# Optimization experiments

Measured on AMD Instinct MI355X. Metric: run time of the kernel, lower is better.

The kernel has to match this reference:

```python
import jax, jax.numpy as jnp
import numpy as np

TOPK = 20

def setup_inputs() -> dict:
    key = jax.random.key(0)
    k1, k2, k3 = jax.random.split(key, 3)
    B, n, D = 4, 4096, 256
    src1 = jax.random.normal(k1, (B, n, D), dtype=jnp.float32)
    src2 = jax.random.normal(k2, (B, n, D), dtype=jnp.float32)
    memoryMartix = jax.random.normal(k3, (n, n), dtype=jnp.float32)
    return {"src1": src1, "src2": src2, "memoryMartix": memoryMartix}

def reference(src1, src2, memoryMartix):
    # softmax over dim=1 of the [n, n] memory matrix
    probs = jax.nn.softmax(memoryMartix, axis=1)            # [n, n]
    # top-k along dim=1: values and indices per row
    vtopk, ind = jax.lax.top_k(probs, TOPK)                 # [n, k], [n, k]
    # gather src2 rows per output position: [B, n, k, D]
    gathered = jnp.take(src2, ind, axis=1)
    # weighted sum over the k selected neighbors
    src = jnp.einsum('bnkd,nk->bnd', gathered, vtopk)       # [B, n, D]
    return src + src1
```

## Files before the change

kernel.cpp:

```cpp
#include <hip/hip_runtime.h>
#include <math.h>

#define TOPK  20
#define NROW  4096
#define DDIM  256
#define NB    4
#define NCHUNK 16

#define AWPB   2
#define ABLOCK (AWPB * 64)
#define BBLOCK 256

typedef float vf4 __attribute__((ext_vector_type(4)));

__device__ __forceinline__ void wave_lds_fence() {
    asm volatile("s_waitcnt lgkmcnt(0)" ::: "memory");
}

__device__ __forceinline__ bool lex_gt(float av, int ai, float bv, int bi) {
    return (av > bv) || (av == bv && ai < bi);
}

__device__ __forceinline__ void bitonic64_desc(float& v, int& i, int lane) {
#pragma unroll
    for (int k = 2; k <= 64; k <<= 1) {
#pragma unroll
        for (int j = k >> 1; j > 0; j >>= 1) {
            float pv = __shfl_xor(v, j, 64);
            int   pi = __shfl_xor(i, j, 64);
            bool takeBig = ((lane & k) == 0) == ((lane & j) == 0);
            bool pBig = lex_gt(pv, pi, v, i);
            if (takeBig == pBig) { v = pv; i = pi; }
        }
    }
}

__global__ __launch_bounds__(ABLOCK, 4) void topk_select(
    const float* __restrict__ mem,
    float* __restrict__ ws_w,
    int*   __restrict__ ws_i)
{
    __shared__ float cand_v[AWPB][64];
    __shared__ int   cand_i[AWPB][64];
    const int wave = threadIdx.x >> 6;
    const int lane = threadIdx.x & 63;
    const int n    = blockIdx.x * AWPB + wave;

    const float4* mrow = (const float4*)(mem + (size_t)n * NROW);
    float4 v4[NCHUNK];
#pragma unroll
    for (int j = 0; j < NCHUNK; ++j) v4[j] = mrow[lane + 64 * j];

    float bv = -INFINITY; int bi = 0x7fffffff;
#pragma unroll
    for (int j = 0; j < NCHUNK; ++j) {
        const int base = 4 * lane + 256 * j;
        if (v4[j].x > bv) { bv = v4[j].x; bi = base + 0; }
        if (v4[j].y > bv) { bv = v4[j].y; bi = base + 1; }
        if (v4[j].z > bv) { bv = v4[j].z; bi = base + 2; }
        if (v4[j].w > bv) { bv = v4[j].w; bi = base + 3; }
    }

    float sv = bv; int si = bi;
    bitonic64_desc(sv, si, lane);
    const float rowmax = __shfl(sv, 0, 64);
    const float tv     = __shfl(sv, 19, 64);
    const int   ti     = __shfl(si, 19, 64);

    float lsum = 0.f;
#pragma unroll
    for (int j = 0; j < NCHUNK; ++j) {
        lsum += __expf(v4[j].x - rowmax) + __expf(v4[j].y - rowmax)
              + __expf(v4[j].z - rowmax) + __expf(v4[j].w - rowmax);
    }
#pragma unroll
    for (int o = 32; o > 0; o >>= 1) lsum += __shfl_xor(lsum, o, 64);
    const float inv_denom = 1.0f / lsum;

    int cnt = 0;
#pragma unroll
    for (int j = 0; j < NCHUNK; ++j) {
        const int base = 4 * lane + 256 * j;
        cnt += (v4[j].x > tv) || (v4[j].x == tv && (base + 0) <= ti);
        cnt += (v4[j].y > tv) || (v4[j].y == tv && (base + 1) <= ti);
        cnt += (v4[j].z > tv) || (v4[j].z == tv && (base + 2) <= ti);
        cnt += (v4[j].w > tv) || (v4[j].w == tv && (base + 3) <= ti);
    }
    int incl = cnt;
#pragma unroll
    for (int o = 1; o < 64; o <<= 1) {
        int t = __shfl_up(incl, o, 64);
        if (lane >= o) incl += t;
    }
    const int total = __builtin_amdgcn_readfirstlane(__shfl(incl, 63, 64));

    float* gw = ws_w + (size_t)n * TOPK;
    int*   gi = ws_i + (size_t)n * TOPK;

    if (total <= 64) {
        int off = incl - cnt;
#pragma unroll
        for (int j = 0; j < NCHUNK; ++j) {
            const int base = 4 * lane + 256 * j;
            const float4 q = v4[j];
            if ((q.x > tv) || (q.x == tv && (base + 0) <= ti)) { cand_v[wave][off] = q.x; cand_i[wave][off] = base + 0; ++off; }
            if ((q.y > tv) || (q.y == tv && (base + 1) <= ti)) { cand_v[wave][off] = q.y; cand_i[wave][off] = base + 1; ++off; }
            if ((q.z > tv) || (q.z == tv && (base + 2) <= ti)) { cand_v[wave][off] = q.z; cand_i[wave][off] = base + 2; ++off; }
            if ((q.w > tv) || (q.w == tv && (base + 3) <= ti)) { cand_v[wave][off] = q.w; cand_i[wave][off] = base + 3; ++off; }
        }
        wave_lds_fence();
        float cv = -INFINITY; int ci = 0x7fffffff;
        if (lane < total) { cv = cand_v[wave][lane]; ci = cand_i[wave][lane]; }
        bitonic64_desc(cv, ci, lane);
        if (lane < TOPK) {
            gw[lane] = __expf(cv - rowmax) * inv_denom;
            gi[lane] = ci;
        }
    } else {
        unsigned long long dead = 0;
        float cv = bv; int ci = bi;
        for (int r = 0; r < TOPK; ++r) {
            float wv = cv; int wi = ci;
#pragma unroll
            for (int o = 32; o > 0; o >>= 1) {
                float ov = __shfl_xor(wv, o, 64);
                int   oi = __shfl_xor(wi, o, 64);
                if (lex_gt(ov, oi, wv, wi)) { wv = ov; wi = oi; }
            }
            if (lane == 0) {
                gw[r] = __expf(wv - rowmax) * inv_denom;
                gi[r] = wi;
            }
            if (ci == wi) {
                const int e = 4 * ((wi >> 8) & 15) + (wi & 3);
                dead |= (1ull << e);
                cv = -INFINITY; ci = 0x7fffffff;
#pragma unroll
                for (int j = 0; j < NCHUNK; ++j) {
                    const int base = 4 * lane + 256 * j;
                    if (!((dead >> (4 * j + 0)) & 1) && v4[j].x > cv) { cv = v4[j].x; ci = base + 0; }
                    if (!((dead >> (4 * j + 1)) & 1) && v4[j].y > cv) { cv = v4[j].y; ci = base + 1; }
                    if (!((dead >> (4 * j + 2)) & 1) && v4[j].z > cv) { cv = v4[j].z; ci = base + 2; }
                    if (!((dead >> (4 * j + 3)) & 1) && v4[j].w > cv) { cv = v4[j].w; ci = base + 3; }
                }
            }
        }
    }
}

__global__ __launch_bounds__(BBLOCK, 4) void gather_epilogue(
    const float* __restrict__ src1,
    const float* __restrict__ src2,
    const float* __restrict__ ws_w,
    const int*   __restrict__ ws_i,
    float* __restrict__ out)
{
    const int bid    = blockIdx.x;
    const int b      = (bid & 7) >> 1;
    const int ngroup = ((bid >> 3) << 1) | (bid & 1);
    const int wave   = threadIdx.x >> 6;
    const int lane   = threadIdx.x & 63;
    const int n      = ngroup * 4 + wave;

    const float* gw = ws_w + (size_t)n * TOPK;
    const int*   gi = ws_i + (size_t)n * TOPK;
    float wk[TOPK]; int ik[TOPK];
#pragma unroll
    for (int k = 0; k < TOPK; ++k) { wk[k] = gw[k]; ik[k] = gi[k]; }

    const vf4* s1  = (const vf4*)src1;
    const vf4* s2b = (const vf4*)src2 + (size_t)b * NROW * (DDIM / 4);
    vf4*       o4  = (vf4*)out;

    const size_t rowbase = ((size_t)b * NROW + n) * (DDIM / 4) + lane;
    vf4 acc = __builtin_nontemporal_load(s1 + rowbase);
#pragma unroll
    for (int k = 0; k < TOPK; ++k) {
        const vf4 g = s2b[(size_t)ik[k] * (DDIM / 4) + lane];
        acc += wk[k] * g;
    }
    __builtin_nontemporal_store(acc, o4 + rowbase);
}

extern "C" void kernel_launch(void* const* d_in, const int* in_sizes, int n_in,
                              void* d_out, int out_size, void* d_ws, size_t ws_size,
                              hipStream_t stream) {
    const float* src1 = (const float*)d_in[0];
    const float* src2 = (const float*)d_in[1];
    const float* mem  = (const float*)d_in[2];
    float* out = (float*)d_out;

    float* ws_w = (float*)d_ws;
    int*   ws_i = (int*)d_ws + (size_t)NROW * TOPK;

    topk_select<<<NROW / AWPB, ABLOCK, 0, stream>>>(mem, ws_w, ws_i);
    gather_epilogue<<<NROW, BBLOCK, 0, stream>>>(src1, src2, ws_w, ws_i, out);
}
```

Before: 152.5 us.

## Split each top-k row across two waves and merge partial results

Each row of the memory matrix is now processed by two waves, each handling half the row. Each wave computes a local max, sum of exps and top-20 candidates, then merges them through shared memory with an online-softmax combine and a final bitonic sort. This halves per-thread register footprint and doubles wave-level parallelism for the select kernel, raising occupancy and memory-level parallelism. The cost is a block barrier and an extra merge sort per row.

```diff
diff --git a/kernel.cpp b/kernel.cpp
--- a/kernel.cpp
+++ b/kernel.cpp
@@ -5,17 +5,12 @@
 #define NROW  4096
 #define DDIM  256
 #define NB    4
-#define NCHUNK 16
-
-#define AWPB   2
-#define ABLOCK (AWPB * 64)
+
+#define HCHUNK 8
+#define ABLOCK 256
 #define BBLOCK 256
 
 typedef float vf4 __attribute__((ext_vector_type(4)));
-
-__device__ __forceinline__ void wave_lds_fence() {
-    asm volatile("s_waitcnt lgkmcnt(0)" ::: "memory");
-}
 
 __device__ __forceinline__ bool lex_gt(float av, int ai, float bv, int bi) {
     return (av > bv) || (av == bv && ai < bi);
@@ -35,26 +30,33 @@
     }
 }
 
-__global__ __launch_bounds__(ABLOCK, 4) void topk_select(
+__global__ __launch_bounds__(ABLOCK, 6) void topk_select(
     const float* __restrict__ mem,
     float* __restrict__ ws_w,
     int*   __restrict__ ws_i)
 {
-    __shared__ float cand_v[AWPB][64];
-    __shared__ int   cand_i[AWPB][64];
-    const int wave = threadIdx.x >> 6;
-    const int lane = threadIdx.x & 63;
-    const int n    = blockIdx.x * AWPB + wave;
-
-    const float4* mrow = (const float4*)(mem + (size_t)n * NROW);
-    float4 v4[NCHUNK];
-#pragma unroll
-    for (int j = 0; j < NCHUNK; ++j) v4[j] = mrow[lane + 64 * j];
+    __shared__ float mv[2][2][TOPK];
+    __shared__ int   mi[2][2][TOPK];
+    __shared__ float mstat[2][2][2];
+    __shared__ float cand_v[4][64];
+    __shared__ int   cand_i[4][64];
+
+    const int wave   = threadIdx.x >> 6;
+    const int lane   = threadIdx.x & 63;
+    const int rowloc = wave >> 1;
+    const int half   = wave & 1;
+    const int n      = blockIdx.x * 2 + rowloc;
+    const int off    = half * (NROW / 2);
+
+    const float4* hrow = (const float4*)(mem + (size_t)n * NROW + off);
+    float4 v4[HCHUNK];
+#pragma unroll
+    for (int j = 0; j < HCHUNK; ++j) v4[j] = hrow[lane + 64 * j];
 
     float bv = -INFINITY; int bi = 0x7fffffff;
 #pragma unroll
-    for (int j = 0; j < NCHUNK; ++j) {
-        const int base = 4 * lane + 256 * j;
+    for (int j = 0; j < HCHUNK; ++j) {
+        const int base = off + 4 * lane + 256 * j;
         if (v4[j].x > bv) { bv = v4[j].x; bi = base + 0; }
         if (v4[j].y > bv) { bv = v4[j].y; bi = base + 1; }
         if (v4[j].z > bv) { bv = v4[j].z; bi = base + 2; }
@@ -63,24 +65,23 @@
 
     float sv = bv; int si = bi;
     bitonic64_desc(sv, si, lane);
-    const float rowmax = __shfl(sv, 0, 64);
-    const float tv     = __shfl(sv, 19, 64);
-    const int   ti     = __shfl(si, 19, 64);
+    const float hmax = __shfl(sv, 0, 64);
+    const float tv   = __shfl(sv, 19, 64);
+    const int   ti   = __shfl(si, 19, 64);
 
     float lsum = 0.f;
 #pragma unroll
-    for (int j = 0; j < NCHUNK; ++j) {
-        lsum += __expf(v4[j].x - rowmax) + __expf(v4[j].y - rowmax)
-              + __expf(v4[j].z - rowmax) + __expf(v4[j].w - rowmax);
+    for (int j = 0; j < HCHUNK; ++j) {
+        lsum += __expf(v4[j].x - hmax) + __expf(v4[j].y - hmax)
+              + __expf(v4[j].z - hmax) + __expf(v4[j].w - hmax);
     }
 #pragma unroll
     for (int o = 32; o > 0; o >>= 1) lsum += __shfl_xor(lsum, o, 64);
-    const float inv_denom = 1.0f / lsum;
 
     int cnt = 0;
 #pragma unroll
-    for (int j = 0; j < NCHUNK; ++j) {
-        const int base = 4 * lane + 256 * j;
+    for (int j = 0; j < HCHUNK; ++j) {
+        const int base = off + 4 * lane + 256 * j;
         cnt += (v4[j].x > tv) || (v4[j].x == tv && (base + 0) <= ti);
         cnt += (v4[j].y > tv) || (v4[j].y == tv && (base + 1) <= ti);
         cnt += (v4[j].z > tv) || (v4[j].z == tv && (base + 2) <= ti);
@@ -94,30 +95,24 @@
     }
     const int total = __builtin_amdgcn_readfirstlane(__shfl(incl, 63, 64));
 
-    float* gw = ws_w + (size_t)n * TOPK;
-    int*   gi = ws_i + (size_t)n * TOPK;
-
     if (total <= 64) {
-        int off = incl - cnt;
-#pragma unroll
-        for (int j = 0; j < NCHUNK; ++j) {
-            const int base = 4 * lane + 256 * j;
+        int o2 = incl - cnt;
+#pragma unroll
+        for (int j = 0; j < HCHUNK; ++j) {
+            const int base = off + 4 * lane + 256 * j;
             const float4 q = v4[j];
-            if ((q.x > tv) || (q.x == tv && (base + 0) <= ti)) { cand_v[wave][off] = q.x; cand_i[wave][off] = base + 0; ++off; }
-            if ((q.y > tv) || (q.y == tv && (base + 1) <= ti)) { cand_v[wave][off] = q.y; cand_i[wave][off] = base + 1; ++off; }
-            if ((q.z > tv) || (q.z == tv && (base + 2) <= ti)) { cand_v[wave][off] = q.z; cand_i[wave][off] = base + 2; ++off; }
-            if ((q.w > tv) || (q.w == tv && (base + 3) <= ti)) { cand_v[wave][off] = q.w; cand_i[wave][off] = base + 3; ++off; }
-        }
-        wave_lds_fence();
+            if ((q.x > tv) || (q.x == tv && (base + 0) <= ti)) { cand_v[wave][o2] = q.x; cand_i[wave][o2] = base + 0; ++o2; }
+            if ((q.y > tv) || (q.y == tv && (base + 1) <= ti)) { cand_v[wave][o2] = q.y; cand_i[wave][o2] = base + 1; ++o2; }
+            if ((q.z > tv) || (q.z == tv && (base + 2) <= ti)) { cand_v[wave][o2] = q.z; cand_i[wave][o2] = base + 2; ++o2; }
+            if ((q.w > tv) || (q.w == tv && (base + 3) <= ti)) { cand_v[wave][o2] = q.w; cand_i[wave][o2] = base + 3; ++o2; }
+        }
+        asm volatile("s_waitcnt lgkmcnt(0)" ::: "memory");
         float cv = -INFINITY; int ci = 0x7fffffff;
         if (lane < total) { cv = cand_v[wave][lane]; ci = cand_i[wave][lane]; }
         bitonic64_desc(cv, ci, lane);
-        if (lane < TOPK) {
-            gw[lane] = __expf(cv - rowmax) * inv_denom;
-            gi[lane] = ci;
-        }
+        if (lane < TOPK) { mv[rowloc][half][lane] = cv; mi[rowloc][half][lane] = ci; }
     } else {
-        unsigned long long dead = 0;
+        unsigned dead = 0;
         float cv = bv; int ci = bi;
         for (int r = 0; r < TOPK; ++r) {
             float wv = cv; int wi = ci;
@@ -127,23 +122,44 @@
                 int   oi = __shfl_xor(wi, o, 64);
                 if (lex_gt(ov, oi, wv, wi)) { wv = ov; wi = oi; }
             }
-            if (lane == 0) {
-                gw[r] = __expf(wv - rowmax) * inv_denom;
-                gi[r] = wi;
-            }
+            if (lane == 0) { mv[rowloc][half][r] = wv; mi[rowloc][half][r] = wi; }
             if (ci == wi) {
-                const int e = 4 * ((wi >> 8) & 15) + (wi & 3);
-                dead |= (1ull << e);
+                const int local = wi - off;
+                dead |= (1u << (4 * (local >> 8) + (local & 3)));
                 cv = -INFINITY; ci = 0x7fffffff;
 #pragma unroll
-                for (int j = 0; j < NCHUNK; ++j) {
-                    const int base = 4 * lane + 256 * j;
+                for (int j = 0; j < HCHUNK; ++j) {
+                    const int base = off + 4 * lane + 256 * j;
                     if (!((dead >> (4 * j + 0)) & 1) && v4[j].x > cv) { cv = v4[j].x; ci = base + 0; }
                     if (!((dead >> (4 * j + 1)) & 1) && v4[j].y > cv) { cv = v4[j].y; ci = base + 1; }
                     if (!((dead >> (4 * j + 2)) & 1) && v4[j].z > cv) { cv = v4[j].z; ci = base + 2; }
                     if (!((dead >> (4 * j + 3)) & 1) && v4[j].w > cv) { cv = v4[j].w; ci = base + 3; }
                 }
             }
+        }
+    }
+    if (lane == 0) { mstat[rowloc][half][0] = hmax; mstat[rowloc][half][1] = lsum; }
+    __syncthreads();
+
+    if (half == 0) {
+        float cv = -INFINITY; int ci = 0x7fffffff;
+        if (lane < 2 * TOPK) {
+            const int h = lane >= TOPK;
+            const int k = h ? lane - TOPK : lane;
+            cv = mv[rowloc][h][k];
+            ci = mi[rowloc][h][k];
+        }
+        bitonic64_desc(cv, ci, lane);
+
+        const float m0 = mstat[rowloc][0][0], s0 = mstat[rowloc][0][1];
+        const float m1 = mstat[rowloc][1][0], s1 = mstat[rowloc][1][1];
+        const float M  = fmaxf(m0, m1);
+        const float S  = s0 * __expf(m0 - M) + s1 * __expf(m1 - M);
+        const float invS = 1.0f / S;
+
+        if (lane < TOPK) {
+            ws_w[(size_t)n * TOPK + lane] = __expf(cv - M) * invS;
+            ws_i[(size_t)n * TOPK + lane] = ci;
         }
     }
 }
@@ -193,6 +209,6 @@
     float* ws_w = (float*)d_ws;
     int*   ws_i = (int*)d_ws + (size_t)NROW * TOPK;
 
-    topk_select<<<NROW / AWPB, ABLOCK, 0, stream>>>(mem, ws_w, ws_i);
+    topk_select<<<NROW / 2, ABLOCK, 0, stream>>>(mem, ws_w, ws_i);
     gather_epilogue<<<NROW, BBLOCK, 0, stream>>>(src1, src2, ws_w, ws_i, out);
 }
```

Result: slower. 170.7 us (+11.9%).
